# Kernel optimization log

Measured on AMD Instinct MI355X. Metric: run time of the kernel, lower is better.

The kernel has to match this reference:

```python
import jax, jax.numpy as jnp
import numpy as np

# config (matches SS2Dv2 defaults: d_model=96, d_state=16, ssm_ratio=2.0, dt_rank=auto=6, k_group=4)
DM, DI, N, K, R = 96, 192, 16, 4, 6
BSZ, H_, W_ = 1, 56, 56


def setup_inputs() -> dict:
    key = jax.random.key(0)
    ks = jax.random.split(key, 8)
    return {
        "x": jax.random.normal(ks[0], (BSZ, H_, W_, DM), jnp.float32),
        "in_proj_w": jax.random.normal(ks[1], (2 * DI, DM), jnp.float32) / np.sqrt(DM).astype(np.float32),
        "conv_w": jax.random.normal(ks[2], (DI, 1, 3, 3), jnp.float32) * 0.1,
        "conv_b": jnp.zeros((DI,), jnp.float32),
        "x_proj_w": jax.random.normal(ks[3], (K, R + 2 * N, DI), jnp.float32) / np.sqrt(DI).astype(np.float32),
        "dt_projs_w": 0.1 * jax.random.uniform(ks[4], (K, DI, R), jnp.float32),
        "dt_projs_bias": 0.1 * jax.random.uniform(ks[5], (K, DI), jnp.float32),
        "A_logs": jnp.zeros((K * DI, N), jnp.float32),
        "Ds": jnp.ones((K * DI,), jnp.float32),
        "ln_w": jnp.ones((DI,), jnp.float32),
        "ln_b": jnp.zeros((DI,), jnp.float32),
        "out_proj_w": jax.random.normal(ks[6], (DM, DI), jnp.float32) / np.sqrt(DI).astype(np.float32),
    }


def _cross_scan(x):
    # x: (B, D, H, W) -> (B, 4, D, L); dirs: row-major, col-major, and their flips
    B, D, H, W = x.shape
    L = H * W
    x0 = x.reshape(B, D, L)
    x1 = jnp.swapaxes(x, 2, 3).reshape(B, D, L)
    return jnp.stack([x0, x1, x0[..., ::-1], x1[..., ::-1]], axis=1)


def _cross_merge(ys, H, W):
    # ys: (B, K, D, L) -> (B, D, L); invert each scan direction and sum
    B, Kk, D, L = ys.shape
    y0 = ys[:, 0]
    y2 = ys[:, 2][..., ::-1]
    y1 = jnp.swapaxes(ys[:, 1].reshape(B, D, W, H), 2, 3).reshape(B, D, L)
    y3 = jnp.swapaxes(ys[:, 3][..., ::-1].reshape(B, D, W, H), 2, 3).reshape(B, D, L)
    return y0 + y1 + y2 + y3


def _forward(x, in_proj_w, conv_w, conv_b, x_proj_w, dt_projs_w, dt_projs_bias,
             A_logs, Ds, ln_w, ln_b, out_proj_w):
    B, H, W, _ = x.shape
    L = H * W
    # in_proj + gate split (channel_first=False -> last dim)
    xz = jnp.einsum('bhwc,oc->bhwo', x, in_proj_w)
    xc, z = jnp.split(xz, 2, axis=-1)
    z = jax.nn.silu(z)
    # depthwise conv (NCHW)
    xc = jnp.transpose(xc, (0, 3, 1, 2))
    xc = jax.lax.conv_general_dilated(
        xc, conv_w, (1, 1), 'SAME', feature_group_count=DI,
        dimension_numbers=('NCHW', 'OIHW', 'NCHW')) + conv_b[None, :, None, None]
    xc = jax.nn.silu(xc)
    # 4-directional cross scan
    xs = _cross_scan(xc)  # (B,K,D,L)
    # grouped x_proj: per direction D -> R+2N
    x_dbl = jnp.einsum('bkdl,krd->bkrl', xs, x_proj_w)
    dts, Bs, Cs = jnp.split(x_dbl, [R, R + N], axis=2)  # (B,K,R,L),(B,K,N,L),(B,K,N,L)
    # grouped dt proj: per direction R -> D
    dts = jnp.einsum('bkrl,kdr->bkdl', dts, dt_projs_w)
    A = -jnp.exp(A_logs.astype(jnp.float32)).reshape(K, DI, N)
    delta = jax.nn.softplus(dts + dt_projs_bias[None, :, :, None])  # (B,K,D,L)
    # S6 selective scan: h_t = exp(delta*A)*h_{t-1} + delta*B*u, y_t = C.h_t + D*u
    dA = jnp.exp(jnp.einsum('bkdl,kdn->bkdln', delta, A))
    dBu = jnp.einsum('bkdl,bknl,bkdl->bkdln', delta, Bs, xs)

    def comb(e1, e2):
        a1, b1 = e1
        a2, b2 = e2
        return a2 * a1, a2 * b1 + b2

    _, h = jax.lax.associative_scan(comb, (dA, dBu), axis=3)  # (B,K,D,L,N)
    y = jnp.einsum('bkdln,bknl->bkdl', h, Cs) + Ds.reshape(K, DI)[None, :, :, None] * xs
    y = _cross_merge(y, H, W).reshape(B, DI, H, W)
    # out_norm: LayerNorm over channels (channel_first=False path)
    y = jnp.transpose(y, (0, 2, 3, 1))  # (B,H,W,D)
    mu = y.mean(-1, keepdims=True)
    var = ((y - mu) ** 2).mean(-1, keepdims=True)
    y = (y - mu) / jnp.sqrt(var + 1e-5) * ln_w + ln_b
    y = y * z
    return jnp.einsum('bhwd,od->bhwo', y, out_proj_w)


def reference(x, in_proj_w, conv_w, conv_b, x_proj_w, dt_projs_w, dt_projs_bias,
              A_logs, Ds, ln_w, ln_b, out_proj_w):
    return _forward(x, in_proj_w, conv_w, conv_b, x_proj_w, dt_projs_w, dt_projs_bias,
                    A_logs, Ds, ln_w, ln_b, out_proj_w)
```

## Files before the change

kernel.cpp:

```cpp
#include <hip/hip_runtime.h>
#include <hip/hip_bf16.h>
#include <math.h>

#define DM 96
#define DI 192
#define NS 16
#define KK 4
#define RR 6
#define HH 56
#define WW 56
#define LL (HH*WW)
#define RN (RR + 2*NS)
#define NCH 64
#define CLL (LL/NCH)

__device__ __forceinline__ float silu_f(float x) { return x / (1.f + __expf(-x)); }
__device__ __forceinline__ float softplus_f(float x) {
    return (x > 20.f) ? x : log1pf(__expf(x));
}

__global__ __launch_bounds__(256) void k_inproj(
        const float* __restrict__ x, const float* __restrict__ w,
        float* __restrict__ xc_t, float* __restrict__ z_nat) {
    __shared__ float xt[32 * 100];
    __shared__ float wt[32 * 100];
    const int l0 = blockIdx.x * 32;
    const int o0 = blockIdx.y * 32;
    const int tid = threadIdx.x;
    for (int i = tid; i < 32 * 24; i += 256) {
        int r = i / 24, q = i % 24;
        *(float4*)&xt[r * 100 + 4 * q] = *(const float4*)&x[(size_t)(l0 + r) * DM + 4 * q];
        *(float4*)&wt[r * 100 + 4 * q] = *(const float4*)&w[(size_t)(o0 + r) * DM + 4 * q];
    }
    __syncthreads();
    const int tx = tid & 15, ty = tid >> 4;
    float acc[2][2] = {};
    for (int c = 0; c < 96; c += 4) {
        float4 av[2], bv[2];
#pragma unroll
        for (int i = 0; i < 2; ++i) av[i] = *(const float4*)&xt[(ty + 16 * i) * 100 + c];
#pragma unroll
        for (int j = 0; j < 2; ++j) bv[j] = *(const float4*)&wt[(tx + 16 * j) * 100 + c];
#pragma unroll
        for (int i = 0; i < 2; ++i)
#pragma unroll
            for (int j = 0; j < 2; ++j) {
                acc[i][j] = fmaf(av[i].x, bv[j].x, acc[i][j]);
                acc[i][j] = fmaf(av[i].y, bv[j].y, acc[i][j]);
                acc[i][j] = fmaf(av[i].z, bv[j].z, acc[i][j]);
                acc[i][j] = fmaf(av[i].w, bv[j].w, acc[i][j]);
            }
    }
    __syncthreads();
    float* ot = xt;
#pragma unroll
    for (int j = 0; j < 2; ++j)
#pragma unroll
        for (int i = 0; i < 2; ++i)
            ot[(tx + 16 * j) * 65 + (ty + 16 * i)] = acc[i][j];
    __syncthreads();
    if (o0 < DI) {
        for (int i = tid; i < 32 * 32; i += 256) {
            int ol = i >> 5, ll = i & 31;
            xc_t[(size_t)(o0 + ol) * LL + l0 + ll] = ot[ol * 65 + ll];
        }
    } else {
        for (int i = tid; i < 32 * 32; i += 256) {
            int ll = i >> 5, ol = i & 31;
            z_nat[(size_t)(l0 + ll) * DI + (o0 - DI) + ol] = silu_f(ot[ol * 65 + ll]);
        }
    }
}

__global__ __launch_bounds__(256) void k_convT(
        const float* __restrict__ xc_t, const float* __restrict__ cw,
        const float* __restrict__ cb, float* __restrict__ xconv, float* __restrict__ xs1) {
    __shared__ float in_s[16 * 56];
    __shared__ float out_s[14 * 57];
    const int d = blockIdx.x;
    const int h0 = blockIdx.y * 14;
    const int tid = threadIdx.x;
    const float* in = xc_t + (size_t)d * LL;
    for (int i = tid; i < 16 * 14; i += 256) {
        int row = i / 14, q = i % 14;
        int r = row - 1 + h0;
        float4 v = make_float4(0.f, 0.f, 0.f, 0.f);
        if (r >= 0 && r < HH) v = *(const float4*)&in[r * WW + 4 * q];
        *(float4*)&in_s[row * 56 + 4 * q] = v;
    }
    __syncthreads();
    const float b0 = cb[d];
    float w9[9];
#pragma unroll
    for (int i = 0; i < 9; ++i) w9[i] = cw[d * 9 + i];
    for (int i = tid; i < 14 * 56; i += 256) {
        int hh = i / 56, w = i % 56;
        float acc = b0;
#pragma unroll
        for (int di = 0; di < 3; ++di)
#pragma unroll
            for (int dj = 0; dj < 3; ++dj) {
                int w2 = w + dj - 1;
                if (w2 < 0 || w2 >= WW) continue;
                acc = fmaf(in_s[(hh + di) * 56 + w2], w9[di * 3 + dj], acc);
            }
        acc = silu_f(acc);
        xconv[(size_t)d * LL + (h0 + hh) * WW + w] = acc;
        out_s[hh * 57 + w] = acc;
    }
    __syncthreads();
    for (int i = tid; i < 14 * 56; i += 256) {
        int w = i / 14, hh = i % 14;
        xs1[(size_t)d * LL + w * HH + h0 + hh] = out_s[hh * 57 + w];
    }
}

__global__ __launch_bounds__(256) void k_xdblD(
        const float* __restrict__ xconv, const float* __restrict__ xs1,
        const float* __restrict__ pw, const float* __restrict__ dtw,
        const float* __restrict__ dtb,
        float* __restrict__ Bn, float* __restrict__ Cn, float* __restrict__ delta) {
    __shared__ float xt[DI * 16];
    __shared__ float wk_s[32 * DI];
    __shared__ float dtS[RR * 17];
    const int k = blockIdx.y;
    const int l0 = blockIdx.x * 16;
    const int tid = threadIdx.x;
    const float* in = (k & 1) ? xs1 : xconv;
    const float* wk = pw + (size_t)k * RN * DI;
    for (int i = tid; i < DI * 4; i += 256) {
        int d = i >> 2, q = i & 3;
        *(float4*)&xt[(d << 4) + 4 * q] = *(const float4*)&in[(size_t)d * LL + l0 + 4 * q];
    }
    {
        const float4* src = (const float4*)(wk + RR * DI);
        float4* dst = (float4*)wk_s;
        for (int i = tid; i < (32 * DI) / 4; i += 256) dst[i] = src[i];
    }
    __syncthreads();
    if (tid < RR * 16) {
        int r = tid >> 4, lx = tid & 15;
        const float* wr = wk + r * DI;
        float acc = 0.f;
#pragma unroll 8
        for (int d = 0; d < DI; ++d) acc = fmaf(xt[(d << 4) + lx], wr[d], acc);
        dtS[r * 17 + lx] = acc;
    }
    {
        const int sx = tid & 15, cg = tid >> 4;
        float acc2[2] = {};
        for (int d = 0; d < DI; d += 4) {
            float x0 = xt[(d + 0) * 16 + sx];
            float x1 = xt[(d + 1) * 16 + sx];
            float x2 = xt[(d + 2) * 16 + sx];
            float x3 = xt[(d + 3) * 16 + sx];
#pragma unroll
            for (int j = 0; j < 2; ++j) {
                float4 wv = *(const float4*)&wk_s[(cg + 16 * j) * DI + d];
                acc2[j] = fmaf(x0, wv.x, acc2[j]);
                acc2[j] = fmaf(x1, wv.y, acc2[j]);
                acc2[j] = fmaf(x2, wv.z, acc2[j]);
                acc2[j] = fmaf(x3, wv.w, acc2[j]);
            }
        }
        int s = l0 + sx;
        Bn[((size_t)k * LL + s) * NS + cg] = acc2[0];
        Cn[((size_t)k * LL + s) * NS + cg] = acc2[1];
    }
    __syncthreads();
    for (int oi = tid; oi < DI * 16; oi += 256) {
        int d = oi >> 4, sl = oi & 15;
        int kd = k * DI + d;
        const float* wr = dtw + (size_t)kd * RR;
        float acc = dtb[kd];
#pragma unroll
        for (int r = 0; r < RR; ++r) acc = fmaf(dtS[r * 17 + sl], wr[r], acc);
        delta[(size_t)kd * LL + l0 + sl] = softplus_f(acc);
    }
}

template<int STP, bool TRANS>
__device__ __forceinline__ void scan_dir(
        const float* __restrict__ pd, const float* __restrict__ pu,
        const float* __restrict__ pB, const float* __restrict__ pC,
        float An0, float An1, float Dv, int c, int n,
        float* __restrict__ sP, float* __restrict__ sH,
        float* __restrict__ yo0,
        float* __restrict__ ysm,
        int im0) {
    float sd = 0.f, h0 = 0.f, h1 = 0.f;
#pragma unroll 7
    for (int tl = 0; tl < CLL; ++tl) {
        float dl = pd[STP * tl];
        float u  = pu[STP * tl];
        float B0 = pB[STP * NS * tl];
        float B1 = pB[STP * NS * tl + 8];
        float dA0 = __expf(dl * An0);
        float dA1 = __expf(dl * An1);
        float du = dl * u;
        h0 = fmaf(dA0, h0, du * B0);
        h1 = fmaf(dA1, h1, du * B1);
        sd += dl;
    }
    sP[c * NS + n]     = __expf(sd * An0);
    sP[c * NS + n + 8] = __expf(sd * An1);
    sH[c * NS + n]     = h0;
    sH[c * NS + n + 8] = h1;
    __syncthreads();
    float hin0 = 0.f, hin1 = 0.f;
    for (int cc = 0; cc < c; ++cc) {
        hin0 = fmaf(sP[cc * NS + n],     hin0, sH[cc * NS + n]);
        hin1 = fmaf(sP[cc * NS + n + 8], hin1, sH[cc * NS + n + 8]);
    }

    float h20 = hin0, h21 = hin1;
    float yreg[7];
#pragma unroll 7
    for (int tl = 0; tl < CLL; ++tl) {
        float dl = pd[STP * tl];
        float u  = pu[STP * tl];
        float B0 = pB[STP * NS * tl];
        float B1 = pB[STP * NS * tl + 8];
        float C0 = pC[STP * NS * tl];
        float C1 = pC[STP * NS * tl + 8];
        float dA0 = __expf(dl * An0);
        float dA1 = __expf(dl * An1);
        float du = dl * u;
        h20 = fmaf(dA0, h20, du * B0);
        h21 = fmaf(dA1, h21, du * B1);
        float acc = h20 * C0 + h21 * C1;
        acc += __shfl_xor(acc, 4, 64);
        acc += __shfl_xor(acc, 2, 64);
        acc += __shfl_xor(acc, 1, 64);
        acc = fmaf(Dv, u, acc);
        if ((tl & 7) == n) yreg[tl >> 3] = acc;
    }
    if (!TRANS) {
#pragma unroll
        for (int j = 0; j < 6; ++j)
            yo0[STP * (j * 8 + n)] = yreg[j];
        if (n == 0)
            yo0[STP * 48] = yreg[6];
    } else {
#pragma unroll
        for (int j = 0; j < 6; ++j) {
            int im = im0 + STP * (j * 8 + n);
            int w = im / HH, hh = im - w * HH;
            ysm[hh * 57 + w] = yreg[j];
        }
        if (n == 0) {
            int im = im0 + STP * 48;
            int w = im / HH, hh = im - w * HH;
            ysm[hh * 57 + w] = yreg[6];
        }
    }
}

__global__ __launch_bounds__(512) void k_scan(
        const float* __restrict__ delta, const float* __restrict__ Bn,
        const float* __restrict__ Cn,
        const float* __restrict__ xconv, const float* __restrict__ xs1,
        const float* __restrict__ A_logs, const float* __restrict__ Ds,
        float* __restrict__ y4) {
    __shared__ float sP[NCH * NS];
    __shared__ float sH[NCH * NS];
    __shared__ float ys[HH * 57];
    int b = blockIdx.x;
    int k = b / DI, d = b % DI;
    int tid = threadIdx.x;
    int c = tid >> 3, n = tid & 7;
    int kd = k * DI + d;
    float An0 = -__expf(A_logs[kd * NS + n]);
    float An1 = -__expf(A_logs[kd * NS + n + 8]);
    float Dv = Ds[kd];
    const float* del = delta + (size_t)kd * LL;
    const float* uP  = ((k & 1) ? xs1 : xconv) + (size_t)d * LL;
    const float* Bb  = Bn + (size_t)k * LL * NS;
    const float* Cb  = Cn + (size_t)k * LL * NS;
    float* yo = y4 + (size_t)kd * LL;
    const int t0 = c * CLL;
    const int imF = t0;
    const int imR = LL - 1 - t0;
    if (k == 0) {
        scan_dir<1, false>(del + imF, uP + imF,
                           Bb + (size_t)imF * NS + n, Cb + (size_t)imF * NS + n,
                           An0, An1, Dv, c, n, sP, sH, yo + imF, nullptr, 0);
    } else if (k == 1) {
        scan_dir<1, true>(del + imF, uP + imF,
                          Bb + (size_t)imF * NS + n, Cb + (size_t)imF * NS + n,
                          An0, An1, Dv, c, n, sP, sH, nullptr, ys, imF);
    } else if (k == 2) {
        scan_dir<-1, false>(del + imR, uP + imR,
                            Bb + (size_t)imR * NS + n, Cb + (size_t)imR * NS + n,
                            An0, An1, Dv, c, n, sP, sH, yo + imR, nullptr, 0);
    } else {
        scan_dir<-1, true>(del + imR, uP + imR,
                           Bb + (size_t)imR * NS + n, Cb + (size_t)imR * NS + n,
                           An0, An1, Dv, c, n, sP, sH, nullptr, ys, imR);
    }
    if (k & 1) {
        __syncthreads();
        for (int p = tid; p < LL; p += 512)
            yo[p] = ys[p + p / WW];
    }
}

__global__ __launch_bounds__(256) void k_lnout(
        const float* __restrict__ y4, const float* __restrict__ z_nat,
        const float* __restrict__ lnw, const float* __restrict__ lnb,
        const float* __restrict__ ow, float* __restrict__ out) {
    __shared__ float yv[16 * 196];
    __shared__ float ow_s[48 * 196];
    __shared__ float mean_s[16], inv_s[16];
    const int l0 = blockIdx.x * 16;
    const int tid = threadIdx.x;
    for (int i = tid; i < DI * 4; i += 256) {
        int d = i >> 2, q = i & 3;
        size_t off = (size_t)d * LL + l0 + 4 * q;
        float4 a = *(const float4*)&y4[off];
        float4 b = *(const float4*)&y4[(size_t)DI * LL + off];
        float4 c2 = *(const float4*)&y4[(size_t)(2 * DI) * LL + off];
        float4 e = *(const float4*)&y4[(size_t)(3 * DI) * LL + off];
        int p = 4 * q;
        yv[(p + 0) * 196 + d] = a.x + b.x + c2.x + e.x;
        yv[(p + 1) * 196 + d] = a.y + b.y + c2.y + e.y;
        yv[(p + 2) * 196 + d] = a.z + b.z + c2.z + e.z;
        yv[(p + 3) * 196 + d] = a.w + b.w + c2.w + e.w;
    }
    __syncthreads();
    {
        int p = tid >> 4, e = tid & 15;
        float s1 = 0.f;
#pragma unroll
        for (int m = 0; m < 12; ++m) s1 += yv[p * 196 + e + 16 * m];
        s1 += __shfl_xor(s1, 8, 64);
        s1 += __shfl_xor(s1, 4, 64);
        s1 += __shfl_xor(s1, 2, 64);
        s1 += __shfl_xor(s1, 1, 64);
        float mean = s1 * (1.f / DI);
        float s2 = 0.f;
#pragma unroll
        for (int m = 0; m < 12; ++m) {
            float dv = yv[p * 196 + e + 16 * m] - mean;
            s2 = fmaf(dv, dv, s2);
        }
        s2 += __shfl_xor(s2, 8, 64);
        s2 += __shfl_xor(s2, 4, 64);
        s2 += __shfl_xor(s2, 2, 64);
        s2 += __shfl_xor(s2, 1, 64);
        if (e == 0) {
            mean_s[p] = mean;
            inv_s[p] = rsqrtf(s2 * (1.f / DI) + 1e-5f);
        }
    }
    __syncthreads();
    for (int i = tid; i < 16 * 48; i += 256) {
        int p = i / 48, q = i % 48;
        float4 z4 = *(const float4*)&z_nat[(size_t)(l0 + p) * DI + 4 * q];
        float4 w4 = *(const float4*)&lnw[4 * q];
        float4 b4 = *(const float4*)&lnb[4 * q];
        float4 yy = *(const float4*)&yv[p * 196 + 4 * q];
        float m = mean_s[p], iv = inv_s[p];
        yy.x = ((yy.x - m) * iv * w4.x + b4.x) * z4.x;
        yy.y = ((yy.y - m) * iv * w4.y + b4.y) * z4.y;
        yy.z = ((yy.z - m) * iv * w4.z + b4.z) * z4.z;
        yy.w = ((yy.w - m) * iv * w4.w + b4.w) * z4.w;
        *(float4*)&yv[p * 196 + 4 * q] = yy;
    }
    const int ty = tid >> 4, tx = tid & 15;
#pragma unroll
    for (int pass = 0; pass < 2; ++pass) {
        __syncthreads();
        for (int i = tid; i < 48 * 48; i += 256) {
            int o = i / 48, q = i % 48;
            *(float4*)&ow_s[o * 196 + 4 * q] =
                *(const float4*)&ow[(size_t)(pass * 48 + o) * DI + 4 * q];
        }
        __syncthreads();
        float acc[3] = {};
        for (int dd = 0; dd < DI; dd += 4) {
            float4 a0 = *(const float4*)&yv[ty * 196 + dd];
#pragma unroll
            for (int j = 0; j < 3; ++j) {
                float4 bv = *(const float4*)&ow_s[(tx + 16 * j) * 196 + dd];
                acc[j] += a0.x * bv.x + a0.y * bv.y + a0.z * bv.z + a0.w * bv.w;
            }
        }
#pragma unroll
        for (int j = 0; j < 3; ++j)
            out[(size_t)(l0 + ty) * DM + pass * 48 + tx + 16 * j] = acc[j];
    }
}

extern "C" void kernel_launch(void* const* d_in, const int* in_sizes, int n_in,
                              void* d_out, int out_size, void* d_ws, size_t ws_size,
                              hipStream_t stream) {
    const float* x    = (const float*)d_in[0];
    const float* ipw  = (const float*)d_in[1];
    const float* cw   = (const float*)d_in[2];
    const float* cb   = (const float*)d_in[3];
    const float* xpw  = (const float*)d_in[4];
    const float* dtw  = (const float*)d_in[5];
    const float* dtb  = (const float*)d_in[6];
    const float* alog = (const float*)d_in[7];
    const float* Dsp  = (const float*)d_in[8];
    const float* lnw  = (const float*)d_in[9];
    const float* lnb  = (const float*)d_in[10];
    const float* ow   = (const float*)d_in[11];
    float* out = (float*)d_out;

    float* ws     = (float*)d_ws;
    float* xc_t   = ws;
    float* z_nat  = xc_t + DI * LL;
    float* xconv  = z_nat + DI * LL;
    float* xs1    = xconv + DI * LL;
    float* Bn     = xs1 + DI * LL;
    float* Cn     = Bn + (size_t)KK * LL * NS;
    float* delta  = Cn + (size_t)KK * LL * NS;
    float* y4     = delta + (size_t)KK * DI * LL;

    k_inproj <<<dim3(LL / 32, 12), 256, 0, stream>>>(x, ipw, xc_t, z_nat);
    k_convT  <<<dim3(DI, 4), 256, 0, stream>>>(xc_t, cw, cb, xconv, xs1);
    k_xdblD  <<<dim3(LL / 16, KK), 256, 0, stream>>>(xconv, xs1, xpw, dtw, dtb, Bn, Cn, delta);
    k_scan   <<<KK * DI, 512, 0, stream>>>(delta, Bn, Cn, xconv, xs1, alog, Dsp, y4);
    k_lnout  <<<LL / 16, 256, 0, stream>>>(y4, z_nat, lnw, lnb, ow, out);
}
```

Before: 176.5 us.

## Fuse all five stages into one cooperative persistent kernel with grid syncs

Replaces the five separate launches (in-proj, depthwise conv, x/dt projection, selective scan, layernorm+out-proj) with a single cooperative kernel of 768 blocks that runs each stage in turn, separated by grid.sync(). The goal is to remove the per-launch overhead and inter-kernel gaps, which matter for a workload this small. Some stages are re-tiled to fit the fixed block count, for example 64-row in-proj tiles and one 32-column B/C projection per thread. The old multi-kernel path stays as a fallback if the cooperative launch fails. The trade-off is grid-wide barrier cost, blocks sitting idle in stages that need fewer than 768, and occupancy limited by 512-thread blocks with about 50KB of shared memory each.

```diff
diff --git a/kernel.cpp b/kernel.cpp
--- a/kernel.cpp
+++ b/kernel.cpp
@@ -1,6 +1,9 @@
 #include <hip/hip_runtime.h>
 #include <hip/hip_bf16.h>
+#include <hip/hip_cooperative_groups.h>
 #include <math.h>
+
+namespace cg = cooperative_groups;
 
 #define DM 96
 #define DI 192
@@ -19,175 +22,13 @@
     return (x > 20.f) ? x : log1pf(__expf(x));
 }
 
-__global__ __launch_bounds__(256) void k_inproj(
-        const float* __restrict__ x, const float* __restrict__ w,
-        float* __restrict__ xc_t, float* __restrict__ z_nat) {
-    __shared__ float xt[32 * 100];
-    __shared__ float wt[32 * 100];
-    const int l0 = blockIdx.x * 32;
-    const int o0 = blockIdx.y * 32;
-    const int tid = threadIdx.x;
-    for (int i = tid; i < 32 * 24; i += 256) {
-        int r = i / 24, q = i % 24;
-        *(float4*)&xt[r * 100 + 4 * q] = *(const float4*)&x[(size_t)(l0 + r) * DM + 4 * q];
-        *(float4*)&wt[r * 100 + 4 * q] = *(const float4*)&w[(size_t)(o0 + r) * DM + 4 * q];
-    }
-    __syncthreads();
-    const int tx = tid & 15, ty = tid >> 4;
-    float acc[2][2] = {};
-    for (int c = 0; c < 96; c += 4) {
-        float4 av[2], bv[2];
-#pragma unroll
-        for (int i = 0; i < 2; ++i) av[i] = *(const float4*)&xt[(ty + 16 * i) * 100 + c];
-#pragma unroll
-        for (int j = 0; j < 2; ++j) bv[j] = *(const float4*)&wt[(tx + 16 * j) * 100 + c];
-#pragma unroll
-        for (int i = 0; i < 2; ++i)
-#pragma unroll
-            for (int j = 0; j < 2; ++j) {
-                acc[i][j] = fmaf(av[i].x, bv[j].x, acc[i][j]);
-                acc[i][j] = fmaf(av[i].y, bv[j].y, acc[i][j]);
-                acc[i][j] = fmaf(av[i].z, bv[j].z, acc[i][j]);
-                acc[i][j] = fmaf(av[i].w, bv[j].w, acc[i][j]);
-            }
-    }
-    __syncthreads();
-    float* ot = xt;
-#pragma unroll
-    for (int j = 0; j < 2; ++j)
-#pragma unroll
-        for (int i = 0; i < 2; ++i)
-            ot[(tx + 16 * j) * 65 + (ty + 16 * i)] = acc[i][j];
-    __syncthreads();
-    if (o0 < DI) {
-        for (int i = tid; i < 32 * 32; i += 256) {
-            int ol = i >> 5, ll = i & 31;
-            xc_t[(size_t)(o0 + ol) * LL + l0 + ll] = ot[ol * 65 + ll];
-        }
-    } else {
-        for (int i = tid; i < 32 * 32; i += 256) {
-            int ll = i >> 5, ol = i & 31;
-            z_nat[(size_t)(l0 + ll) * DI + (o0 - DI) + ol] = silu_f(ot[ol * 65 + ll]);
-        }
-    }
-}
-
-__global__ __launch_bounds__(256) void k_convT(
-        const float* __restrict__ xc_t, const float* __restrict__ cw,
-        const float* __restrict__ cb, float* __restrict__ xconv, float* __restrict__ xs1) {
-    __shared__ float in_s[16 * 56];
-    __shared__ float out_s[14 * 57];
-    const int d = blockIdx.x;
-    const int h0 = blockIdx.y * 14;
-    const int tid = threadIdx.x;
-    const float* in = xc_t + (size_t)d * LL;
-    for (int i = tid; i < 16 * 14; i += 256) {
-        int row = i / 14, q = i % 14;
-        int r = row - 1 + h0;
-        float4 v = make_float4(0.f, 0.f, 0.f, 0.f);
-        if (r >= 0 && r < HH) v = *(const float4*)&in[r * WW + 4 * q];
-        *(float4*)&in_s[row * 56 + 4 * q] = v;
-    }
-    __syncthreads();
-    const float b0 = cb[d];
-    float w9[9];
-#pragma unroll
-    for (int i = 0; i < 9; ++i) w9[i] = cw[d * 9 + i];
-    for (int i = tid; i < 14 * 56; i += 256) {
-        int hh = i / 56, w = i % 56;
-        float acc = b0;
-#pragma unroll
-        for (int di = 0; di < 3; ++di)
-#pragma unroll
-            for (int dj = 0; dj < 3; ++dj) {
-                int w2 = w + dj - 1;
-                if (w2 < 0 || w2 >= WW) continue;
-                acc = fmaf(in_s[(hh + di) * 56 + w2], w9[di * 3 + dj], acc);
-            }
-        acc = silu_f(acc);
-        xconv[(size_t)d * LL + (h0 + hh) * WW + w] = acc;
-        out_s[hh * 57 + w] = acc;
-    }
-    __syncthreads();
-    for (int i = tid; i < 14 * 56; i += 256) {
-        int w = i / 14, hh = i % 14;
-        xs1[(size_t)d * LL + w * HH + h0 + hh] = out_s[hh * 57 + w];
-    }
-}
-
-__global__ __launch_bounds__(256) void k_xdblD(
-        const float* __restrict__ xconv, const float* __restrict__ xs1,
-        const float* __restrict__ pw, const float* __restrict__ dtw,
-        const float* __restrict__ dtb,
-        float* __restrict__ Bn, float* __restrict__ Cn, float* __restrict__ delta) {
-    __shared__ float xt[DI * 16];
-    __shared__ float wk_s[32 * DI];
-    __shared__ float dtS[RR * 17];
-    const int k = blockIdx.y;
-    const int l0 = blockIdx.x * 16;
-    const int tid = threadIdx.x;
-    const float* in = (k & 1) ? xs1 : xconv;
-    const float* wk = pw + (size_t)k * RN * DI;
-    for (int i = tid; i < DI * 4; i += 256) {
-        int d = i >> 2, q = i & 3;
-        *(float4*)&xt[(d << 4) + 4 * q] = *(const float4*)&in[(size_t)d * LL + l0 + 4 * q];
-    }
-    {
-        const float4* src = (const float4*)(wk + RR * DI);
-        float4* dst = (float4*)wk_s;
-        for (int i = tid; i < (32 * DI) / 4; i += 256) dst[i] = src[i];
-    }
-    __syncthreads();
-    if (tid < RR * 16) {
-        int r = tid >> 4, lx = tid & 15;
-        const float* wr = wk + r * DI;
-        float acc = 0.f;
-#pragma unroll 8
-        for (int d = 0; d < DI; ++d) acc = fmaf(xt[(d << 4) + lx], wr[d], acc);
-        dtS[r * 17 + lx] = acc;
-    }
-    {
-        const int sx = tid & 15, cg = tid >> 4;
-        float acc2[2] = {};
-        for (int d = 0; d < DI; d += 4) {
-            float x0 = xt[(d + 0) * 16 + sx];
-            float x1 = xt[(d + 1) * 16 + sx];
-            float x2 = xt[(d + 2) * 16 + sx];
-            float x3 = xt[(d + 3) * 16 + sx];
-#pragma unroll
-            for (int j = 0; j < 2; ++j) {
-                float4 wv = *(const float4*)&wk_s[(cg + 16 * j) * DI + d];
-                acc2[j] = fmaf(x0, wv.x, acc2[j]);
-                acc2[j] = fmaf(x1, wv.y, acc2[j]);
-                acc2[j] = fmaf(x2, wv.z, acc2[j]);
-                acc2[j] = fmaf(x3, wv.w, acc2[j]);
-            }
-        }
-        int s = l0 + sx;
-        Bn[((size_t)k * LL + s) * NS + cg] = acc2[0];
-        Cn[((size_t)k * LL + s) * NS + cg] = acc2[1];
-    }
-    __syncthreads();
-    for (int oi = tid; oi < DI * 16; oi += 256) {
-        int d = oi >> 4, sl = oi & 15;
-        int kd = k * DI + d;
-        const float* wr = dtw + (size_t)kd * RR;
-        float acc = dtb[kd];
-#pragma unroll
-        for (int r = 0; r < RR; ++r) acc = fmaf(dtS[r * 17 + sl], wr[r], acc);
-        delta[(size_t)kd * LL + l0 + sl] = softplus_f(acc);
-    }
-}
-
 template<int STP, bool TRANS>
 __device__ __forceinline__ void scan_dir(
         const float* __restrict__ pd, const float* __restrict__ pu,
         const float* __restrict__ pB, const float* __restrict__ pC,
         float An0, float An1, float Dv, int c, int n,
         float* __restrict__ sP, float* __restrict__ sH,
-        float* __restrict__ yo0,
-        float* __restrict__ ysm,
-        int im0) {
+        float* __restrict__ yo0, float* __restrict__ ysm, int im0) {
     float sd = 0.f, h0 = 0.f, h1 = 0.f;
 #pragma unroll 7
     for (int tl = 0; tl < CLL; ++tl) {
@@ -212,7 +53,6 @@
         hin0 = fmaf(sP[cc * NS + n],     hin0, sH[cc * NS + n]);
         hin1 = fmaf(sP[cc * NS + n + 8], hin1, sH[cc * NS + n + 8]);
     }
-
     float h20 = hin0, h21 = hin1;
     float yreg[7];
 #pragma unroll 7
@@ -253,6 +93,457 @@
             int w = im / HH, hh = im - w * HH;
             ysm[hh * 57 + w] = yreg[6];
         }
+    }
+}
+
+__global__ __launch_bounds__(512, 6) void k_fused(
+        const float* __restrict__ x, const float* __restrict__ ipw,
+        const float* __restrict__ cw, const float* __restrict__ cb,
+        const float* __restrict__ xpw, const float* __restrict__ dtw,
+        const float* __restrict__ dtb, const float* __restrict__ alog,
+        const float* __restrict__ Dsp, const float* __restrict__ lnw,
+        const float* __restrict__ lnb, const float* __restrict__ ow,
+        float* __restrict__ out,
+        float* __restrict__ xc_t, float* __restrict__ z_nat,
+        float* __restrict__ xconv, float* __restrict__ xs1,
+        float* __restrict__ Bn, float* __restrict__ Cn,
+        float* __restrict__ delta, float* __restrict__ y4) {
+    cg::grid_group grid = cg::this_grid();
+    __shared__ __align__(16) float sm[12608];
+    const int gid = blockIdx.x;
+    const int tid = threadIdx.x;
+
+    if (gid < 588) {
+        const int to = gid / 49, tl = gid % 49;
+        const int l0 = tl * 64, o0 = to * 32;
+        float* xt = sm;
+        float* wt = sm + 6400;
+        for (int i = tid; i < 64 * 24; i += 512) {
+            int r = i / 24, q = i % 24;
+            *(float4*)&xt[r * 100 + 4 * q] = *(const float4*)&x[(size_t)(l0 + r) * DM + 4 * q];
+        }
+        for (int i = tid; i < 32 * 24; i += 512) {
+            int r = i / 24, q = i % 24;
+            *(float4*)&wt[r * 100 + 4 * q] = *(const float4*)&ipw[(size_t)(o0 + r) * DM + 4 * q];
+        }
+        __syncthreads();
+        const int tx = tid & 15, ty = tid >> 4;
+        float acc[2][2] = {};
+        for (int c = 0; c < 96; c += 4) {
+            float4 a0 = *(const float4*)&xt[ty * 100 + c];
+            float4 a1 = *(const float4*)&xt[(ty + 32) * 100 + c];
+            float4 b0 = *(const float4*)&wt[tx * 100 + c];
+            float4 b1 = *(const float4*)&wt[(tx + 16) * 100 + c];
+            acc[0][0] += a0.x * b0.x + a0.y * b0.y + a0.z * b0.z + a0.w * b0.w;
+            acc[0][1] += a0.x * b1.x + a0.y * b1.y + a0.z * b1.z + a0.w * b1.w;
+            acc[1][0] += a1.x * b0.x + a1.y * b0.y + a1.z * b0.z + a1.w * b0.w;
+            acc[1][1] += a1.x * b1.x + a1.y * b1.y + a1.z * b1.z + a1.w * b1.w;
+        }
+        __syncthreads();
+        float* ot = xt;
+        ot[tx * 65 + ty]             = acc[0][0];
+        ot[tx * 65 + ty + 32]        = acc[1][0];
+        ot[(tx + 16) * 65 + ty]      = acc[0][1];
+        ot[(tx + 16) * 65 + ty + 32] = acc[1][1];
+        __syncthreads();
+        if (o0 < DI) {
+            for (int i = tid; i < 32 * 64; i += 512) {
+                int ol = i >> 6, ll = i & 63;
+                xc_t[(size_t)(o0 + ol) * LL + l0 + ll] = ot[ol * 65 + ll];
+            }
+        } else {
+            for (int i = tid; i < 32 * 64; i += 512) {
+                int ll = i >> 5, ol = i & 31;
+                z_nat[(size_t)(l0 + ll) * DI + (o0 - DI) + ol] = silu_f(ot[ol * 65 + ll]);
+            }
+        }
+    }
+    grid.sync();
+
+    {
+        const int d = gid >> 2;
+        const int h0 = (gid & 3) * 14;
+        float* in_s = sm;
+        float* out_s = sm + 896;
+        const float* in = xc_t + (size_t)d * LL;
+        for (int i = tid; i < 16 * 14; i += 512) {
+            int row = i / 14, q = i % 14;
+            int r = row - 1 + h0;
+            float4 v = make_float4(0.f, 0.f, 0.f, 0.f);
+            if (r >= 0 && r < HH) v = *(const float4*)&in[r * WW + 4 * q];
+            *(float4*)&in_s[row * 56 + 4 * q] = v;
+        }
+        __syncthreads();
+        const float b0 = cb[d];
+        float w9[9];
+#pragma unroll
+        for (int i = 0; i < 9; ++i) w9[i] = cw[d * 9 + i];
+        for (int i = tid; i < 14 * 56; i += 512) {
+            int hh = i / 56, w = i % 56;
+            float acc = b0;
+#pragma unroll
+            for (int di = 0; di < 3; ++di)
+#pragma unroll
+                for (int dj = 0; dj < 3; ++dj) {
+                    int w2 = w + dj - 1;
+                    if (w2 < 0 || w2 >= WW) continue;
+                    acc = fmaf(in_s[(hh + di) * 56 + w2], w9[di * 3 + dj], acc);
+                }
+            acc = silu_f(acc);
+            xconv[(size_t)d * LL + (h0 + hh) * WW + w] = acc;
+            out_s[hh * 57 + w] = acc;
+        }
+        __syncthreads();
+        for (int i = tid; i < 14 * 56; i += 512) {
+            int w = i / 14, hh = i % 14;
+            xs1[(size_t)d * LL + w * HH + h0 + hh] = out_s[hh * 57 + w];
+        }
+    }
+    grid.sync();
+
+    for (int t = gid; t < 784; t += 768) {
+        const int k = t & 3, lt = t >> 2;
+        const int l0 = lt * 16;
+        const float* in = (k & 1) ? xs1 : xconv;
+        const float* wk = xpw + (size_t)k * RN * DI;
+        float* xt = sm;
+        float* wk_s = sm + 3072;
+        float* dtS = sm + 9344;
+        for (int i = tid; i < DI * 4; i += 512) {
+            int d = i >> 2, q = i & 3;
+            *(float4*)&xt[(d << 4) + 4 * q] = *(const float4*)&in[(size_t)d * LL + l0 + 4 * q];
+        }
+        for (int i = tid; i < 32 * 48; i += 512) {
+            int col = i / 48, q = i % 48;
+            *(float4*)&wk_s[col * 196 + 4 * q] = *(const float4*)&wk[RR * DI + col * DI + 4 * q];
+        }
+        __syncthreads();
+        if (tid < RR * 16) {
+            int r = tid >> 4, lx = tid & 15;
+            const float* wr = wk + r * DI;
+            float acc = 0.f;
+#pragma unroll 8
+            for (int d = 0; d < DI; ++d) acc = fmaf(xt[(d << 4) + lx], wr[d], acc);
+            dtS[r * 17 + lx] = acc;
+        }
+        {
+            const int sx = tid & 15, cg2 = tid >> 4;
+            float a = 0.f;
+            for (int d = 0; d < DI; d += 4) {
+                float x0 = xt[(d + 0) * 16 + sx];
+                float x1 = xt[(d + 1) * 16 + sx];
+                float x2 = xt[(d + 2) * 16 + sx];
+                float x3 = xt[(d + 3) * 16 + sx];
+                float4 wv = *(const float4*)&wk_s[cg2 * 196 + d];
+                a = fmaf(x0, wv.x, a);
+                a = fmaf(x1, wv.y, a);
+                a = fmaf(x2, wv.z, a);
+                a = fmaf(x3, wv.w, a);
+            }
+            int s = l0 + sx;
+            if (cg2 < NS) Bn[((size_t)k * LL + s) * NS + cg2] = a;
+            else          Cn[((size_t)k * LL + s) * NS + (cg2 - NS)] = a;
+        }
+        __syncthreads();
+        for (int oi = tid; oi < DI * 16; oi += 512) {
+            int d = oi >> 4, sl = oi & 15;
+            int kd = k * DI + d;
+            const float* wr = dtw + (size_t)kd * RR;
+            float acc = dtb[kd];
+#pragma unroll
+            for (int r = 0; r < RR; ++r) acc = fmaf(dtS[r * 17 + sl], wr[r], acc);
+            delta[(size_t)kd * LL + l0 + sl] = softplus_f(acc);
+        }
+        __syncthreads();
+    }
+    grid.sync();
+
+    {
+        float* sP = sm;
+        float* sH = sm + 1024;
+        float* ys = sm + 2048;
+        const int k = gid / DI, d = gid % DI;
+        const int c = tid >> 3, n = tid & 7;
+        const int kd = k * DI + d;
+        float An0 = -__expf(alog[kd * NS + n]);
+        float An1 = -__expf(alog[kd * NS + n + 8]);
+        float Dv = Dsp[kd];
+        const float* del = delta + (size_t)kd * LL;
+        const float* uP  = ((k & 1) ? xs1 : xconv) + (size_t)d * LL;
+        const float* Bb  = Bn + (size_t)k * LL * NS;
+        const float* Cb  = Cn + (size_t)k * LL * NS;
+        float* yo = y4 + (size_t)kd * LL;
+        const int t0 = c * CLL;
+        const int imF = t0;
+        const int imR = LL - 1 - t0;
+        if (k == 0) {
+            scan_dir<1, false>(del + imF, uP + imF,
+                               Bb + (size_t)imF * NS + n, Cb + (size_t)imF * NS + n,
+                               An0, An1, Dv, c, n, sP, sH, yo + imF, nullptr, 0);
+        } else if (k == 1) {
+            scan_dir<1, true>(del + imF, uP + imF,
+                              Bb + (size_t)imF * NS + n, Cb + (size_t)imF * NS + n,
+                              An0, An1, Dv, c, n, sP, sH, nullptr, ys, imF);
+        } else if (k == 2) {
+            scan_dir<-1, false>(del + imR, uP + imR,
+                                Bb + (size_t)imR * NS + n, Cb + (size_t)imR * NS + n,
+                                An0, An1, Dv, c, n, sP, sH, yo + imR, nullptr, 0);
+        } else {
+            scan_dir<-1, true>(del + imR, uP + imR,
+                               Bb + (size_t)imR * NS + n, Cb + (size_t)imR * NS + n,
+                               An0, An1, Dv, c, n, sP, sH, nullptr, ys, imR);
+        }
+        if (k & 1) {
+            __syncthreads();
+            for (int p = tid; p < LL; p += 512)
+                yo[p] = ys[p + p / WW];
+        }
+    }
+    grid.sync();
+
+    if (gid < 196) {
+        const int l0 = gid * 16;
+        float* yv = sm;
+        float* ow_s = sm + 3136;
+        float* mean_s = sm + 12544;
+        float* inv_s = sm + 12560;
+        for (int i = tid; i < DI * 4; i += 512) {
+            int d = i >> 2, q = i & 3;
+            size_t off = (size_t)d * LL + l0 + 4 * q;
+            float4 a = *(const float4*)&y4[off];
+            float4 b = *(const float4*)&y4[(size_t)DI * LL + off];
+            float4 c2 = *(const float4*)&y4[(size_t)(2 * DI) * LL + off];
+            float4 e = *(const float4*)&y4[(size_t)(3 * DI) * LL + off];
+            int p = 4 * q;
+            yv[(p + 0) * 196 + d] = a.x + b.x + c2.x + e.x;
+            yv[(p + 1) * 196 + d] = a.y + b.y + c2.y + e.y;
+            yv[(p + 2) * 196 + d] = a.z + b.z + c2.z + e.z;
+            yv[(p + 3) * 196 + d] = a.w + b.w + c2.w + e.w;
+        }
+        __syncthreads();
+        if (tid < 256) {
+            int p = tid >> 4, e = tid & 15;
+            float s1 = 0.f;
+#pragma unroll
+            for (int m = 0; m < 12; ++m) s1 += yv[p * 196 + e + 16 * m];
+            s1 += __shfl_xor(s1, 8, 64);
+            s1 += __shfl_xor(s1, 4, 64);
+            s1 += __shfl_xor(s1, 2, 64);
+            s1 += __shfl_xor(s1, 1, 64);
+            float mean = s1 * (1.f / DI);
+            float s2 = 0.f;
+#pragma unroll
+            for (int m = 0; m < 12; ++m) {
+                float dv = yv[p * 196 + e + 16 * m] - mean;
+                s2 = fmaf(dv, dv, s2);
+            }
+            s2 += __shfl_xor(s2, 8, 64);
+            s2 += __shfl_xor(s2, 4, 64);
+            s2 += __shfl_xor(s2, 2, 64);
+            s2 += __shfl_xor(s2, 1, 64);
+            if (e == 0) {
+                mean_s[p] = mean;
+                inv_s[p] = rsqrtf(s2 * (1.f / DI) + 1e-5f);
+            }
+        }
+        __syncthreads();
+        for (int i = tid; i < 16 * 48; i += 512) {
+            int p = i / 48, q = i % 48;
+            float4 z4 = *(const float4*)&z_nat[(size_t)(l0 + p) * DI + 4 * q];
+            float4 w4 = *(const float4*)&lnw[4 * q];
+            float4 b4 = *(const float4*)&lnb[4 * q];
+            float4 yy = *(const float4*)&yv[p * 196 + 4 * q];
+            float m = mean_s[p], iv = inv_s[p];
+            yy.x = ((yy.x - m) * iv * w4.x + b4.x) * z4.x;
+            yy.y = ((yy.y - m) * iv * w4.y + b4.y) * z4.y;
+            yy.z = ((yy.z - m) * iv * w4.z + b4.z) * z4.z;
+            yy.w = ((yy.w - m) * iv * w4.w + b4.w) * z4.w;
+            *(float4*)&yv[p * 196 + 4 * q] = yy;
+        }
+        const int ty = tid >> 5, tx = tid & 31;
+#pragma unroll
+        for (int pass = 0; pass < 2; ++pass) {
+            __syncthreads();
+            for (int i = tid; i < 48 * 48; i += 512) {
+                int o = i / 48, q = i % 48;
+                *(float4*)&ow_s[o * 196 + 4 * q] =
+                    *(const float4*)&ow[(size_t)(pass * 48 + o) * DI + 4 * q];
+            }
+            __syncthreads();
+#pragma unroll
+            for (int jj = 0; jj < 2; ++jj) {
+                int o = tx + 32 * jj;
+                if (o < 48) {
+                    float a = 0.f;
+                    for (int dd = 0; dd < DI; dd += 4) {
+                        float4 a0 = *(const float4*)&yv[ty * 196 + dd];
+                        float4 bv = *(const float4*)&ow_s[o * 196 + dd];
+                        a += a0.x * bv.x + a0.y * bv.y + a0.z * bv.z + a0.w * bv.w;
+                    }
+                    out[(size_t)(l0 + ty) * DM + pass * 48 + o] = a;
+                }
+            }
+        }
+    }
+}
+
+__global__ __launch_bounds__(256) void k_inproj(
+        const float* __restrict__ x, const float* __restrict__ w,
+        float* __restrict__ xc_t, float* __restrict__ z_nat) {
+    __shared__ float xt[32 * 100];
+    __shared__ float wt[32 * 100];
+    const int l0 = blockIdx.x * 32;
+    const int o0 = blockIdx.y * 32;
+    const int tid = threadIdx.x;
+    for (int i = tid; i < 32 * 24; i += 256) {
+        int r = i / 24, q = i % 24;
+        *(float4*)&xt[r * 100 + 4 * q] = *(const float4*)&x[(size_t)(l0 + r) * DM + 4 * q];
+        *(float4*)&wt[r * 100 + 4 * q] = *(const float4*)&w[(size_t)(o0 + r) * DM + 4 * q];
+    }
+    __syncthreads();
+    const int tx = tid & 15, ty = tid >> 4;
+    float acc[2][2] = {};
+    for (int c = 0; c < 96; c += 4) {
+        float4 av[2], bv[2];
+#pragma unroll
+        for (int i = 0; i < 2; ++i) av[i] = *(const float4*)&xt[(ty + 16 * i) * 100 + c];
+#pragma unroll
+        for (int j = 0; j < 2; ++j) bv[j] = *(const float4*)&wt[(tx + 16 * j) * 100 + c];
+#pragma unroll
+        for (int i = 0; i < 2; ++i)
+#pragma unroll
+            for (int j = 0; j < 2; ++j) {
+                acc[i][j] = fmaf(av[i].x, bv[j].x, acc[i][j]);
+                acc[i][j] = fmaf(av[i].y, bv[j].y, acc[i][j]);
+                acc[i][j] = fmaf(av[i].z, bv[j].z, acc[i][j]);
+                acc[i][j] = fmaf(av[i].w, bv[j].w, acc[i][j]);
+            }
+    }
+    __syncthreads();
+    float* ot = xt;
+#pragma unroll
+    for (int j = 0; j < 2; ++j)
+#pragma unroll
+        for (int i = 0; i < 2; ++i)
+            ot[(tx + 16 * j) * 65 + (ty + 16 * i)] = acc[i][j];
+    __syncthreads();
+    if (o0 < DI) {
+        for (int i = tid; i < 32 * 32; i += 256) {
+            int ol = i >> 5, ll = i & 31;
+            xc_t[(size_t)(o0 + ol) * LL + l0 + ll] = ot[ol * 65 + ll];
+        }
+    } else {
+        for (int i = tid; i < 32 * 32; i += 256) {
+            int ll = i >> 5, ol = i & 31;
+            z_nat[(size_t)(l0 + ll) * DI + (o0 - DI) + ol] = silu_f(ot[ol * 65 + ll]);
+        }
+    }
+}
+
+__global__ __launch_bounds__(256) void k_convT(
+        const float* __restrict__ xc_t, const float* __restrict__ cw,
+        const float* __restrict__ cb, float* __restrict__ xconv, float* __restrict__ xs1) {
+    __shared__ float in_s[16 * 56];
+    __shared__ float out_s[14 * 57];
+    const int d = blockIdx.x;
+    const int h0 = blockIdx.y * 14;
+    const int tid = threadIdx.x;
+    const float* in = xc_t + (size_t)d * LL;
+    for (int i = tid; i < 16 * 14; i += 256) {
+        int row = i / 14, q = i % 14;
+        int r = row - 1 + h0;
+        float4 v = make_float4(0.f, 0.f, 0.f, 0.f);
+        if (r >= 0 && r < HH) v = *(const float4*)&in[r * WW + 4 * q];
+        *(float4*)&in_s[row * 56 + 4 * q] = v;
+    }
+    __syncthreads();
+    const float b0 = cb[d];
+    float w9[9];
+#pragma unroll
+    for (int i = 0; i < 9; ++i) w9[i] = cw[d * 9 + i];
+    for (int i = tid; i < 14 * 56; i += 256) {
+        int hh = i / 56, w = i % 56;
+        float acc = b0;
+#pragma unroll
+        for (int di = 0; di < 3; ++di)
+#pragma unroll
+            for (int dj = 0; dj < 3; ++dj) {
+                int w2 = w + dj - 1;
+                if (w2 < 0 || w2 >= WW) continue;
+                acc = fmaf(in_s[(hh + di) * 56 + w2], w9[di * 3 + dj], acc);
+            }
+        acc = silu_f(acc);
+        xconv[(size_t)d * LL + (h0 + hh) * WW + w] = acc;
+        out_s[hh * 57 + w] = acc;
+    }
+    __syncthreads();
+    for (int i = tid; i < 14 * 56; i += 256) {
+        int w = i / 14, hh = i % 14;
+        xs1[(size_t)d * LL + w * HH + h0 + hh] = out_s[hh * 57 + w];
+    }
+}
+
+__global__ __launch_bounds__(256) void k_xdblD(
+        const float* __restrict__ xconv, const float* __restrict__ xs1,
+        const float* __restrict__ pw, const float* __restrict__ dtw,
+        const float* __restrict__ dtb,
+        float* __restrict__ Bn, float* __restrict__ Cn, float* __restrict__ delta) {
+    __shared__ float xt[DI * 16];
+    __shared__ float wk_s[32 * DI];
+    __shared__ float dtS[RR * 17];
+    const int k = blockIdx.y;
+    const int l0 = blockIdx.x * 16;
+    const int tid = threadIdx.x;
+    const float* in = (k & 1) ? xs1 : xconv;
+    const float* wk = pw + (size_t)k * RN * DI;
+    for (int i = tid; i < DI * 4; i += 256) {
+        int d = i >> 2, q = i & 3;
+        *(float4*)&xt[(d << 4) + 4 * q] = *(const float4*)&in[(size_t)d * LL + l0 + 4 * q];
+    }
+    {
+        const float4* src = (const float4*)(wk + RR * DI);
+        float4* dst = (float4*)wk_s;
+        for (int i = tid; i < (32 * DI) / 4; i += 256) dst[i] = src[i];
+    }
+    __syncthreads();
+    if (tid < RR * 16) {
+        int r = tid >> 4, lx = tid & 15;
+        const float* wr = wk + r * DI;
+        float acc = 0.f;
+#pragma unroll 8
+        for (int d = 0; d < DI; ++d) acc = fmaf(xt[(d << 4) + lx], wr[d], acc);
+        dtS[r * 17 + lx] = acc;
+    }
+    {
+        const int sx = tid & 15, cg = tid >> 4;
+        float acc2[2] = {};
+        for (int d = 0; d < DI; d += 4) {
+            float x0 = xt[(d + 0) * 16 + sx];
+            float x1 = xt[(d + 1) * 16 + sx];
+            float x2 = xt[(d + 2) * 16 + sx];
+            float x3 = xt[(d + 3) * 16 + sx];
+#pragma unroll
+            for (int j = 0; j < 2; ++j) {
+                float4 wv = *(const float4*)&wk_s[(cg + 16 * j) * DI + d];
+                acc2[j] = fmaf(x0, wv.x, acc2[j]);
+                acc2[j] = fmaf(x1, wv.y, acc2[j]);
+                acc2[j] = fmaf(x2, wv.z, acc2[j]);
+                acc2[j] = fmaf(x3, wv.w, acc2[j]);
+            }
+        }
+        int s = l0 + sx;
+        Bn[((size_t)k * LL + s) * NS + cg] = acc2[0];
+        Cn[((size_t)k * LL + s) * NS + cg] = acc2[1];
+    }
+    __syncthreads();
+    for (int oi = tid; oi < DI * 16; oi += 256) {
+        int d = oi >> 4, sl = oi & 15;
+        int kd = k * DI + d;
+        const float* wr = dtw + (size_t)kd * RR;
+        float acc = dtb[kd];
+#pragma unroll
+        for (int r = 0; r < RR; ++r) acc = fmaf(dtS[r * 17 + sl], wr[r], acc);
+        delta[(size_t)kd * LL + l0 + sl] = softplus_f(acc);
     }
 }
 
@@ -419,9 +710,20 @@
     float* delta  = Cn + (size_t)KK * LL * NS;
     float* y4     = delta + (size_t)KK * DI * LL;
 
-    k_inproj <<<dim3(LL / 32, 12), 256, 0, stream>>>(x, ipw, xc_t, z_nat);
-    k_convT  <<<dim3(DI, 4), 256, 0, stream>>>(xc_t, cw, cb, xconv, xs1);
-    k_xdblD  <<<dim3(LL / 16, KK), 256, 0, stream>>>(xconv, xs1, xpw, dtw, dtb, Bn, Cn, delta);
-    k_scan   <<<KK * DI, 512, 0, stream>>>(delta, Bn, Cn, xconv, xs1, alog, Dsp, y4);
-    k_lnout  <<<LL / 16, 256, 0, stream>>>(y4, z_nat, lnw, lnb, ow, out);
-}
+    void* kargs[] = {
+        (void*)&x, (void*)&ipw, (void*)&cw, (void*)&cb, (void*)&xpw,
+        (void*)&dtw, (void*)&dtb, (void*)&alog, (void*)&Dsp, (void*)&lnw,
+        (void*)&lnb, (void*)&ow, (void*)&out,
+        (void*)&xc_t, (void*)&z_nat, (void*)&xconv, (void*)&xs1,
+        (void*)&Bn, (void*)&Cn, (void*)&delta, (void*)&y4
+    };
+    hipError_t err = hipLaunchCooperativeKernel((void*)k_fused, dim3(768), dim3(512),
+                                                kargs, 0, stream);
+    if (err != hipSuccess) {
+        k_inproj <<<dim3(LL / 32, 12), 256, 0, stream>>>(x, ipw, xc_t, z_nat);
+        k_convT  <<<dim3(DI, 4), 256, 0, stream>>>(xc_t, cw, cb, xconv, xs1);
+        k_xdblD  <<<dim3(LL / 16, KK), 256, 0, stream>>>(xconv, xs1, xpw, dtw, dtb, Bn, Cn, delta);
+        k_scan   <<<KK * DI, 512, 0, stream>>>(delta, Bn, Cn, xconv, xs1, alog, Dsp, y4);
+        k_lnout  <<<LL / 16, 256, 0, stream>>>(y4, z_nat, lnw, lnb, ow, out);
+    }
+}
```

New measurement: 549.7 us. 212% more time.

## Fuse in-projection with depthwise conv, one block per output channel

Applied to the files above, without the earlier changes.

Merges the in-projection GEMM and the depthwise 3x3 conv+SiLU into one kernel. Each block computes a full output-channel row (all L positions) into shared memory, then either applies SiLU for the gate or runs the conv and writes both scan layouts. This removes the xc_t round trip through global memory and one launch. The gate is now stored channel-major, and the LayerNorm kernel reads it that way. The trade-offs are only 384 blocks, each rereading the whole input x with a per-thread dot product instead of a tiled GEMM, and a large shared-memory footprint that limits occupancy.

```diff
diff --git a/kernel.cpp b/kernel.cpp
--- a/kernel.cpp
+++ b/kernel.cpp
@@ -19,100 +19,74 @@
     return (x > 20.f) ? x : log1pf(__expf(x));
 }
 
-__global__ __launch_bounds__(256) void k_inproj(
-        const float* __restrict__ x, const float* __restrict__ w,
-        float* __restrict__ xc_t, float* __restrict__ z_nat) {
-    __shared__ float xt[32 * 100];
-    __shared__ float wt[32 * 100];
-    const int l0 = blockIdx.x * 32;
-    const int o0 = blockIdx.y * 32;
+__global__ __launch_bounds__(256) void k_fuse1(
+        const float* __restrict__ x, const float* __restrict__ ipw,
+        const float* __restrict__ cw, const float* __restrict__ cb,
+        float* __restrict__ xconv, float* __restrict__ xs1,
+        float* __restrict__ z_t) {
+    __shared__ float row_s[LL];
+    __shared__ float out_s[HH * 57];
+    const int b = blockIdx.x;
     const int tid = threadIdx.x;
-    for (int i = tid; i < 32 * 24; i += 256) {
-        int r = i / 24, q = i % 24;
-        *(float4*)&xt[r * 100 + 4 * q] = *(const float4*)&x[(size_t)(l0 + r) * DM + 4 * q];
-        *(float4*)&wt[r * 100 + 4 * q] = *(const float4*)&w[(size_t)(o0 + r) * DM + 4 * q];
-    }
-    __syncthreads();
-    const int tx = tid & 15, ty = tid >> 4;
-    float acc[2][2] = {};
-    for (int c = 0; c < 96; c += 4) {
-        float4 av[2], bv[2];
-#pragma unroll
-        for (int i = 0; i < 2; ++i) av[i] = *(const float4*)&xt[(ty + 16 * i) * 100 + c];
-#pragma unroll
-        for (int j = 0; j < 2; ++j) bv[j] = *(const float4*)&wt[(tx + 16 * j) * 100 + c];
-#pragma unroll
-        for (int i = 0; i < 2; ++i)
-#pragma unroll
-            for (int j = 0; j < 2; ++j) {
-                acc[i][j] = fmaf(av[i].x, bv[j].x, acc[i][j]);
-                acc[i][j] = fmaf(av[i].y, bv[j].y, acc[i][j]);
-                acc[i][j] = fmaf(av[i].z, bv[j].z, acc[i][j]);
-                acc[i][j] = fmaf(av[i].w, bv[j].w, acc[i][j]);
-            }
-    }
-    __syncthreads();
-    float* ot = xt;
-#pragma unroll
-    for (int j = 0; j < 2; ++j)
-#pragma unroll
-        for (int i = 0; i < 2; ++i)
-            ot[(tx + 16 * j) * 65 + (ty + 16 * i)] = acc[i][j];
-    __syncthreads();
-    if (o0 < DI) {
-        for (int i = tid; i < 32 * 32; i += 256) {
-            int ol = i >> 5, ll = i & 31;
-            xc_t[(size_t)(o0 + ol) * LL + l0 + ll] = ot[ol * 65 + ll];
-        }
-    } else {
-        for (int i = tid; i < 32 * 32; i += 256) {
-            int ll = i >> 5, ol = i & 31;
-            z_nat[(size_t)(l0 + ll) * DI + (o0 - DI) + ol] = silu_f(ot[ol * 65 + ll]);
-        }
-    }
-}
-
-__global__ __launch_bounds__(256) void k_convT(
-        const float* __restrict__ xc_t, const float* __restrict__ cw,
-        const float* __restrict__ cb, float* __restrict__ xconv, float* __restrict__ xs1) {
-    __shared__ float in_s[16 * 56];
-    __shared__ float out_s[14 * 57];
-    const int d = blockIdx.x;
-    const int h0 = blockIdx.y * 14;
-    const int tid = threadIdx.x;
-    const float* in = xc_t + (size_t)d * LL;
-    for (int i = tid; i < 16 * 14; i += 256) {
-        int row = i / 14, q = i % 14;
-        int r = row - 1 + h0;
-        float4 v = make_float4(0.f, 0.f, 0.f, 0.f);
-        if (r >= 0 && r < HH) v = *(const float4*)&in[r * WW + 4 * q];
-        *(float4*)&in_s[row * 56 + 4 * q] = v;
-    }
-    __syncthreads();
+    const bool zpath = (b >= DI);
+    const int orow = b;
+    const int d = zpath ? (b - DI) : b;
+
+    const int ol = tid >> 2, part = tid & 3;
+    float4 wreg[6];
+    {
+        const float* wr = ipw + (size_t)orow * DM + part * 24;
+#pragma unroll
+        for (int j = 0; j < 6; ++j) wreg[j] = *(const float4*)&wr[4 * j];
+    }
+    for (int t = 0; t < 49; ++t) {
+        int l = t * 64 + ol;
+        const float* xr = x + (size_t)l * DM + part * 24;
+        float acc = 0.f;
+#pragma unroll
+        for (int j = 0; j < 6; ++j) {
+            float4 xv = *(const float4*)&xr[4 * j];
+            acc += xv.x * wreg[j].x + xv.y * wreg[j].y
+                 + xv.z * wreg[j].z + xv.w * wreg[j].w;
+        }
+        acc += __shfl_xor(acc, 1, 64);
+        acc += __shfl_xor(acc, 2, 64);
+        if (part == 0) row_s[l] = acc;
+    }
+    __syncthreads();
+
+    if (zpath) {
+        float* zo = z_t + (size_t)d * LL;
+        for (int i = tid; i < LL; i += 256)
+            zo[i] = silu_f(row_s[i]);
+        return;
+    }
     const float b0 = cb[d];
     float w9[9];
 #pragma unroll
     for (int i = 0; i < 9; ++i) w9[i] = cw[d * 9 + i];
-    for (int i = tid; i < 14 * 56; i += 256) {
-        int hh = i / 56, w = i % 56;
+    for (int i = tid; i < LL; i += 256) {
+        int h = i / WW, w = i % WW;
         float acc = b0;
 #pragma unroll
-        for (int di = 0; di < 3; ++di)
+        for (int di = 0; di < 3; ++di) {
+            int hh = h + di - 1;
+            if (hh < 0 || hh >= HH) continue;
 #pragma unroll
             for (int dj = 0; dj < 3; ++dj) {
                 int w2 = w + dj - 1;
                 if (w2 < 0 || w2 >= WW) continue;
-                acc = fmaf(in_s[(hh + di) * 56 + w2], w9[di * 3 + dj], acc);
+                acc = fmaf(row_s[hh * WW + w2], w9[di * 3 + dj], acc);
             }
+        }
         acc = silu_f(acc);
-        xconv[(size_t)d * LL + (h0 + hh) * WW + w] = acc;
-        out_s[hh * 57 + w] = acc;
-    }
-    __syncthreads();
-    for (int i = tid; i < 14 * 56; i += 256) {
-        int w = i / 14, hh = i % 14;
-        xs1[(size_t)d * LL + w * HH + h0 + hh] = out_s[hh * 57 + w];
-    }
+        xconv[(size_t)d * LL + i] = acc;
+        out_s[h * 57 + w] = acc;
+    }
+    __syncthreads();
+    float* xo = xs1 + (size_t)d * LL;
+    for (int s = tid; s < LL; s += 256)
+        xo[s] = out_s[(s % HH) * 57 + s / HH];
 }
 
 __global__ __launch_bounds__(256) void k_xdblD(
@@ -185,9 +159,7 @@
         const float* __restrict__ pB, const float* __restrict__ pC,
         float An0, float An1, float Dv, int c, int n,
         float* __restrict__ sP, float* __restrict__ sH,
-        float* __restrict__ yo0,
-        float* __restrict__ ysm,
-        int im0) {
+        float* __restrict__ yo0, float* __restrict__ ysm, int im0) {
     float sd = 0.f, h0 = 0.f, h1 = 0.f;
 #pragma unroll 7
     for (int tl = 0; tl < CLL; ++tl) {
@@ -212,7 +184,6 @@
         hin0 = fmaf(sP[cc * NS + n],     hin0, sH[cc * NS + n]);
         hin1 = fmaf(sP[cc * NS + n + 8], hin1, sH[cc * NS + n + 8]);
     }
-
     float h20 = hin0, h21 = hin1;
     float yreg[7];
 #pragma unroll 7
@@ -306,7 +277,7 @@
 }
 
 __global__ __launch_bounds__(256) void k_lnout(
-        const float* __restrict__ y4, const float* __restrict__ z_nat,
+        const float* __restrict__ y4, const float* __restrict__ z_t,
         const float* __restrict__ lnw, const float* __restrict__ lnb,
         const float* __restrict__ ow, float* __restrict__ out) {
     __shared__ float yv[16 * 196];
@@ -354,18 +325,17 @@
         }
     }
     __syncthreads();
-    for (int i = tid; i < 16 * 48; i += 256) {
-        int p = i / 48, q = i % 48;
-        float4 z4 = *(const float4*)&z_nat[(size_t)(l0 + p) * DI + 4 * q];
-        float4 w4 = *(const float4*)&lnw[4 * q];
-        float4 b4 = *(const float4*)&lnb[4 * q];
-        float4 yy = *(const float4*)&yv[p * 196 + 4 * q];
-        float m = mean_s[p], iv = inv_s[p];
-        yy.x = ((yy.x - m) * iv * w4.x + b4.x) * z4.x;
-        yy.y = ((yy.y - m) * iv * w4.y + b4.y) * z4.y;
-        yy.z = ((yy.z - m) * iv * w4.z + b4.z) * z4.z;
-        yy.w = ((yy.w - m) * iv * w4.w + b4.w) * z4.w;
-        *(float4*)&yv[p * 196 + 4 * q] = yy;
+    for (int i = tid; i < DI * 4; i += 256) {
+        int d = i >> 2, q = i & 3;
+        float4 zz = *(const float4*)&z_t[(size_t)d * LL + l0 + 4 * q];
+        float wv = lnw[d], bv = lnb[d];
+        const float zf[4] = {zz.x, zz.y, zz.z, zz.w};
+#pragma unroll
+        for (int j = 0; j < 4; ++j) {
+            int p = 4 * q + j;
+            float yn = (yv[p * 196 + d] - mean_s[p]) * inv_s[p] * wv + bv;
+            yv[p * 196 + d] = yn * zf[j];
+        }
     }
     const int ty = tid >> 4, tx = tid & 15;
 #pragma unroll
@@ -410,18 +380,16 @@
     float* out = (float*)d_out;
 
     float* ws     = (float*)d_ws;
-    float* xc_t   = ws;
-    float* z_nat  = xc_t + DI * LL;
-    float* xconv  = z_nat + DI * LL;
+    float* z_t    = ws;
+    float* xconv  = z_t + DI * LL;
     float* xs1    = xconv + DI * LL;
     float* Bn     = xs1 + DI * LL;
     float* Cn     = Bn + (size_t)KK * LL * NS;
     float* delta  = Cn + (size_t)KK * LL * NS;
     float* y4     = delta + (size_t)KK * DI * LL;
 
-    k_inproj <<<dim3(LL / 32, 12), 256, 0, stream>>>(x, ipw, xc_t, z_nat);
-    k_convT  <<<dim3(DI, 4), 256, 0, stream>>>(xc_t, cw, cb, xconv, xs1);
-    k_xdblD  <<<dim3(LL / 16, KK), 256, 0, stream>>>(xconv, xs1, xpw, dtw, dtb, Bn, Cn, delta);
-    k_scan   <<<KK * DI, 512, 0, stream>>>(delta, Bn, Cn, xconv, xs1, alog, Dsp, y4);
-    k_lnout  <<<LL / 16, 256, 0, stream>>>(y4, z_nat, lnw, lnb, ow, out);
-}
+    k_fuse1 <<<2 * DI, 256, 0, stream>>>(x, ipw, cw, cb, xconv, xs1, z_t);
+    k_xdblD <<<dim3(LL / 16, KK), 256, 0, stream>>>(xconv, xs1, xpw, dtw, dtb, Bn, Cn, delta);
+    k_scan  <<<KK * DI, 512, 0, stream>>>(delta, Bn, Cn, xconv, xs1, alog, Dsp, y4);
+    k_lnout <<<LL / 16, 256, 0, stream>>>(y4, z_t, lnw, lnb, ow, out);
+}
```

Result: slower. 195.4 us (+10.7%).
